# Kernel optimization log

Hardware: AMD Instinct MI355X
Metric: run time of the kernel (lower is better)

## Reference

```python
import jax, jax.numpy as jnp
import numpy as np

EPS = 1e-6
T, B, E, H, D, P = 1024, 4, 512, 8, 64, 64  # tgt_len, bsz, embed_dim, heads, head_dim, proj_dim


def setup_inputs() -> dict:
    key = jax.random.key(0)
    ks = jax.random.split(key, 8)
    wscale = (2.0 / (E + E)) ** 0.5  # xavier-ish, gain=init_scale**-0.5=1
    return {
        "x": jax.random.normal(ks[0], (T, B, E), jnp.float32),
        "random_matrices": jax.random.normal(ks[1], (H, P, D), jnp.float32),
        "Wq": jax.random.normal(ks[2], (E, E), jnp.float32) * wscale,
        "bq": jnp.zeros((E,), jnp.float32),
        "Wk": jax.random.normal(ks[3], (E, E), jnp.float32) * wscale,
        "bk": jnp.zeros((E,), jnp.float32),
        "Wv": jax.random.normal(ks[4], (E, E), jnp.float32) * wscale,
        "bv": jnp.zeros((E,), jnp.float32),
        "Wo": jax.random.normal(ks[5], (E, E), jnp.float32) * wscale,
        "bo": jnp.zeros((E,), jnp.float32),
    }


def _phi(x, rm, tau=1.0):
    # RFA trig random features: l2-normalize (scaled by 1/tau), project with
    # per-head random matrices, then [sin, cos] / sqrt(proj_dim).
    # x: [T,B,H,D], rm: [H,P,D] -> [T,B,H,2P]
    xn = x / (tau * jnp.maximum(jnp.linalg.norm(x, axis=-1, keepdims=True), EPS))
    proj = jnp.einsum('tbhd,hpd->tbhp', xn, rm)
    return jnp.concatenate([jnp.sin(proj), jnp.cos(proj)], axis=-1) * (P ** -0.5)


def reference(x, random_matrices, Wq, bq, Wk, bk, Wv, bv, Wo, bo):
    t, b, e = x.shape
    q = (x @ Wq.T + bq).reshape(t, b, H, D)
    k = (x @ Wk.T + bk).reshape(t, b, H, D)
    v = (x @ Wv.T + bv).reshape(t, b, H, D)

    pq = _phi(q, random_matrices)  # [T,B,H,2P]
    pk = _phi(k, random_matrices)  # [T,B,H,2P]

    K = 2 * P
    s0 = jnp.zeros((b, H, K, D), x.dtype)
    z0 = jnp.zeros((b, H, K), x.dtype)

    def step(carry, inp):
        s, z = carry
        pq_t, pk_t, v_t = inp  # [B,H,K], [B,H,K], [B,H,D]
        s = s + pk_t[..., :, None] * v_t[..., None, :]   # outer(phi_k, v)
        z = z + pk_t
        qs = jnp.einsum('bhk,bhkd->bhd', pq_t, s)
        qz = jnp.maximum(jnp.einsum('bhk,bhk->bh', pq_t, z), EPS)
        return (s, z), qs / qz[..., None]

    _, attn = jax.lax.scan(step, (s0, z0), (pq, pk, v))  # attn: [T,B,H,D]
    attn = attn.reshape(t, b, e)
    return attn @ Wo.T + bo
```

## Files before the change

kernel.cpp:

```cpp
#include <hip/hip_runtime.h>

#define T_ 1024
#define B_ 4
#define E_ 512
#define H_ 8
#define D_ 64
#define P_ 64
#define K2 128
#define N_ (T_*B_)
#define CHK 64
#define NC (T_/CHK)
#define BH (B_*H_)
#define EPSV 1e-6f

typedef unsigned int uint;
typedef unsigned short ushort;
typedef short short8 __attribute__((ext_vector_type(8)));
typedef float f32x4 __attribute__((ext_vector_type(4)));

__device__ __forceinline__ float b2f(ushort u){ return __uint_as_float(((uint)u) << 16); }
__device__ __forceinline__ ushort f2b(float f){
  uint x = __float_as_uint(f);
  return (ushort)((x + 0x7fffu + ((x >> 16) & 1u)) >> 16);
}
__device__ __forceinline__ float lo16(uint u){ return __uint_as_float(u << 16); }
__device__ __forceinline__ float hi16(uint u){ return __uint_as_float(u & 0xffff0000u); }
__device__ __forceinline__ void st(float* p, float v){ *p = v; }
__device__ __forceinline__ void st(ushort* p, float v){ *p = f2b(v); }

__device__ __forceinline__ void gl16(const ushort* g, ushort* lds) {
  __builtin_amdgcn_global_load_lds(
      (const __attribute__((address_space(1))) uint*)g,
      (__attribute__((address_space(3))) uint*)lds, 16, 0, 0);
}

__global__ __launch_bounds__(256) void cast_kernel(
    const float* __restrict__ x, const float* __restrict__ wq, const float* __restrict__ wk,
    const float* __restrict__ wv, const float* __restrict__ wo, const float* __restrict__ rm,
    ushort* __restrict__ xb, ushort* __restrict__ wqb, ushort* __restrict__ wkb,
    ushort* __restrict__ wvb, ushort* __restrict__ wob, ushort* __restrict__ rmb)
{
  const float* src; ushort* dst; int n4;
  switch (blockIdx.y) {
    case 0:  src = x;  dst = xb;  n4 = N_ * E_ / 4; break;
    case 1:  src = wq; dst = wqb; n4 = E_ * E_ / 4; break;
    case 2:  src = wk; dst = wkb; n4 = E_ * E_ / 4; break;
    case 3:  src = wv; dst = wvb; n4 = E_ * E_ / 4; break;
    case 4:  src = wo; dst = wob; n4 = E_ * E_ / 4; break;
    default: src = rm; dst = rmb; n4 = H_ * P_ * D_ / 4; break;
  }
  const int stride = gridDim.x * 256;
  for (int i = blockIdx.x * 256 + threadIdx.x; i < n4; i += stride) {
    const float4 v = *(const float4*)(src + (size_t)i * 4);
    ushort4 o; o.x = f2b(v.x); o.y = f2b(v.y); o.z = f2b(v.z); o.w = f2b(v.w);
    *(ushort4*)(dst + (size_t)i * 4) = o;
  }
}

template<typename OutT>
__device__ __forceinline__ void gemm_tile(
    const ushort* __restrict__ A, const ushort* __restrict__ W,
    const float* __restrict__ bias, OutT* __restrict__ out,
    const int row0, const int col0)
{
  __shared__ ushort sA[128 * 32];
  __shared__ ushort sB[64 * 32];
  const int tid = threadIdx.x, w = tid >> 6, lane = tid & 63;
  const int lrow = lane >> 2, lk8 = (lane & 3) * 8;
  const ushort* gA = A + (size_t)(row0 + w * 16 + lrow) * E_ + lk8;
  const ushort* gB = W + (size_t)(col0 + w * 16 + lrow) * E_ + lk8;
  ushort* lA = sA + w * 512;
  ushort* lB = sB + w * 512;
  const int r = lane & 15, kg = lane >> 4, kq = kg * 8;
  f32x4 acc[4][4] = {};
  for (int k0 = 0; k0 < E_; k0 += 32) {
    gl16(gA + k0,             lA);
    gl16(gA + k0 + 32 * E_,   lA + 1024);
    gl16(gA + k0 + 64 * E_,   lA + 2048);
    gl16(gA + k0 + 96 * E_,   lA + 3072);
    gl16(gB + k0,             lB);
    gl16(gB + k0 + 32 * E_,   lB + 1024);
    __syncthreads();
    short8 af[4], bf[4];
    #pragma unroll
    for (int m = 0; m < 4; ++m) af[m] = *(const short8*)(sA + (w * 64 + m * 16 + r) * 32 + kq);
    #pragma unroll
    for (int n = 0; n < 4; ++n) bf[n] = *(const short8*)(sB + (n * 16 + r) * 32 + kq);
    #pragma unroll
    for (int m = 0; m < 4; ++m)
      #pragma unroll
      for (int n = 0; n < 4; ++n)
        acc[m][n] = __builtin_amdgcn_mfma_f32_16x16x32_bf16(af[m], bf[n], acc[m][n], 0, 0, 0);
    __syncthreads();
  }
  float bs[4];
  #pragma unroll
  for (int n = 0; n < 4; ++n) bs[n] = bias[col0 + n * 16 + r];
  #pragma unroll
  for (int m = 0; m < 4; ++m) {
    #pragma unroll
    for (int j = 0; j < 4; ++j) {
      const int row_g = row0 + w * 64 + m * 16 + kg * 4 + j;
      #pragma unroll
      for (int n = 0; n < 4; ++n)
        st(out + (size_t)row_g * E_ + col0 + n * 16 + r, acc[m][n][j] + bs[n]);
    }
  }
}

__global__ __launch_bounds__(128) void gemm_qkv_kernel(
    const ushort* __restrict__ A,
    const ushort* __restrict__ wq, const ushort* __restrict__ wk, const ushort* __restrict__ wv,
    const float* __restrict__ bq, const float* __restrict__ bk, const float* __restrict__ bv,
    ushort* __restrict__ qb, ushort* __restrict__ kb, ushort* __restrict__ vb)
{
  const ushort* W; const float* bias; ushort* dst;
  if (blockIdx.z == 0)      { W = wq; bias = bq; dst = qb; }
  else if (blockIdx.z == 1) { W = wk; bias = bk; dst = kb; }
  else                      { W = wv; bias = bv; dst = vb; }
  gemm_tile<ushort>(A, W, bias, dst, blockIdx.x * 128, blockIdx.y * 64);
}

__global__ __launch_bounds__(128) void gemm_out_kernel(
    const ushort* __restrict__ A, const ushort* __restrict__ W,
    const float* __restrict__ bias, float* __restrict__ out)
{
  gemm_tile<float>(A, W, bias, out, blockIdx.x * 128, blockIdx.y * 64);
}

__global__ __launch_bounds__(256) void phi_kernel(
    const ushort* __restrict__ qb, const ushort* __restrict__ kb,
    const ushort* __restrict__ rmb, ushort* __restrict__ pq, ushort* __restrict__ pk)
{
  __shared__ ushort xq[64][72];
  __shared__ ushort rms[64][72];
  __shared__ float inv_s[64];
  const int tid = threadIdx.x;
  const int h = blockIdx.y;
  const ushort* src = blockIdx.z ? kb : qb;
  ushort* dst = blockIdx.z ? pk : pq;
  const int n0 = blockIdx.x * 64;
  const int row = tid >> 2, seg = (tid & 3) * 16;
  {
    const ushort* gq = src + (size_t)(n0 + row) * E_ + h * D_ + seg;
    const ushort* gr = rmb + ((size_t)h * P_ + row) * D_ + seg;
    const uint4 q0 = *(const uint4*)(gq);
    const uint4 q1 = *(const uint4*)(gq + 8);
    *(uint4*)(&xq[row][seg])      = q0;
    *(uint4*)(&xq[row][seg + 8])  = q1;
    *(uint4*)(&rms[row][seg])     = *(const uint4*)(gr);
    *(uint4*)(&rms[row][seg + 8]) = *(const uint4*)(gr + 8);
    float s2 = 0.f;
    const uint* qw = (const uint*)&q0;
    #pragma unroll
    for (int i = 0; i < 4; ++i) { const float a = lo16(qw[i]), b = hi16(qw[i]); s2 += a*a + b*b; }
    const uint* qw1 = (const uint*)&q1;
    #pragma unroll
    for (int i = 0; i < 4; ++i) { const float a = lo16(qw1[i]), b = hi16(qw1[i]); s2 += a*a + b*b; }
    s2 += __shfl_xor(s2, 1, 64);
    s2 += __shfl_xor(s2, 2, 64);
    if ((tid & 3) == 0) inv_s[row] = 1.0f / fmaxf(sqrtf(s2), EPSV);
  }
  __syncthreads();
  const int w = tid >> 6, lane = tid & 63;
  const int r = lane & 15, kg = lane >> 4;
  const int m0 = w * 16;
  f32x4 acc[4] = {};
  #pragma unroll
  for (int k0 = 0; k0 < D_; k0 += 32) {
    const short8 a = *(const short8*)(&xq[m0 + r][k0 + kg * 8]);
    #pragma unroll
    for (int nt = 0; nt < 4; ++nt) {
      const short8 bfr = *(const short8*)(&rms[nt * 16 + r][k0 + kg * 8]);
      acc[nt] = __builtin_amdgcn_mfma_f32_16x16x32_bf16(a, bfr, acc[nt], 0, 0, 0);
    }
  }
  #pragma unroll
  for (int j = 0; j < 4; ++j) {
    const int rr = m0 + kg * 4 + j;
    const float inv = inv_s[rr];
    const size_t base = ((size_t)(n0 + rr) * H_ + h) * K2;
    #pragma unroll
    for (int nt = 0; nt < 4; ++nt) {
      const int p = nt * 16 + r;
      const float proj = acc[nt][j] * inv;
      dst[base + p]      = f2b(__sinf(proj) * 0.125f);
      dst[base + 64 + p] = f2b(__cosf(proj) * 0.125f);
    }
  }
}

__global__ __launch_bounds__(256) void chunk_sum_kernel(
    const ushort* __restrict__ pk, const ushort* __restrict__ v,
    float* __restrict__ cS, float* __restrict__ cz)
{
  const int c = blockIdx.x, bh = blockIdx.y, b = bh >> 3, h = bh & 7;
  __shared__ ushort pkT[K2][88];
  __shared__ ushort vT[D_][88];
  const int tid = threadIdx.x;
  for (int i = tid; i < CHK * 16; i += 256) {
    const int tt = i >> 4, k8 = (i & 15) * 8;
    const int n = (c * CHK + tt) * B_ + b;
    const ushort4 u0 = *(const ushort4*)(pk + ((size_t)n * H_ + h) * K2 + k8);
    const ushort4 u1 = *(const ushort4*)(pk + ((size_t)n * H_ + h) * K2 + k8 + 4);
    pkT[k8+0][tt] = u0.x; pkT[k8+1][tt] = u0.y; pkT[k8+2][tt] = u0.z; pkT[k8+3][tt] = u0.w;
    pkT[k8+4][tt] = u1.x; pkT[k8+5][tt] = u1.y; pkT[k8+6][tt] = u1.z; pkT[k8+7][tt] = u1.w;
  }
  for (int i = tid; i < CHK * 16; i += 256) {
    const int tt = i >> 4, d4 = (i & 15) * 4;
    const int n = (c * CHK + tt) * B_ + b;
    const ushort4 u = *(const ushort4*)(v + (size_t)n * E_ + h * D_ + d4);
    vT[d4+0][tt] = u.x; vT[d4+1][tt] = u.y; vT[d4+2][tt] = u.z; vT[d4+3][tt] = u.w;
  }
  __syncthreads();
  const int w = tid >> 6, lane = tid & 63;
  const int r = lane & 15, kb = lane >> 4;
  const int m0 = w * 32;
  f32x4 acc[2][4] = {};
  #pragma unroll
  for (int k0 = 0; k0 < CHK; k0 += 32) {
    const short8 a0 = *(const short8*)(&pkT[m0 + r][k0 + kb * 8]);
    const short8 a1 = *(const short8*)(&pkT[m0 + 16 + r][k0 + kb * 8]);
    #pragma unroll
    for (int nt = 0; nt < 4; ++nt) {
      const short8 bv = *(const short8*)(&vT[nt * 16 + r][k0 + kb * 8]);
      acc[0][nt] = __builtin_amdgcn_mfma_f32_16x16x32_bf16(a0, bv, acc[0][nt], 0, 0, 0);
      acc[1][nt] = __builtin_amdgcn_mfma_f32_16x16x32_bf16(a1, bv, acc[1][nt], 0, 0, 0);
    }
  }
  float* So = cS + (size_t)(c * BH + bh) * (K2 * D_);
  #pragma unroll
  for (int mt = 0; mt < 2; ++mt)
    #pragma unroll
    for (int nt = 0; nt < 4; ++nt)
      #pragma unroll
      for (int j = 0; j < 4; ++j)
        So[(m0 + mt * 16 + kb * 4 + j) * D_ + nt * 16 + r] = acc[mt][nt][j];
  if (tid < K2) {
    float zacc = 0.f;
    #pragma unroll
    for (int i2 = 0; i2 < CHK / 2; ++i2) {
      const uint u = *(const uint*)(&pkT[tid][i2 * 2]);
      zacc += lo16(u) + hi16(u);
    }
    cz[(size_t)(c * BH + bh) * K2 + tid] = zacc;
  }
}

__global__ __launch_bounds__(256) void prefix_kernel(
    float* __restrict__ cS, float* __restrict__ cz)
{
  const int gid = blockIdx.x * 256 + threadIdx.x;
  const int bh = gid >> 13, rem = gid & 8191;
  float run = 0.f;
  #pragma unroll
  for (int c = 0; c < NC; ++c) {
    float* p = cS + (((size_t)(c * BH + bh)) << 13) + rem;
    const float t = *p; *p = run; run += t;
  }
  if (gid < BH * K2) {
    const int zbh = gid >> 7, k2 = gid & 127;
    float rz = 0.f;
    #pragma unroll
    for (int c = 0; c < NC; ++c) {
      float* pz = cz + (size_t)(c * BH + zbh) * K2 + k2;
      const float t = *pz; *pz = rz; rz += t;
    }
  }
}

__global__ __launch_bounds__(256) void chunk_out_kernel(
    const ushort* __restrict__ pq, const ushort* __restrict__ pkg,
    const ushort* __restrict__ v, const float* __restrict__ Sp,
    const float* __restrict__ zp, ushort* __restrict__ attn)
{
  const int c = blockIdx.x, bh = blockIdx.y, b = bh >> 3, h = bh & 7;
  __shared__ ushort pq_s[CHK][136];
  __shared__ ushort pk_s[CHK][136];
  __shared__ ushort SpT_s[D_][136];
  __shared__ ushort vT_s[D_][88];
  __shared__ ushort Am_s[CHK][88];
  __shared__ float zps[K2];
  __shared__ float dens_s[CHK];
  __shared__ float inv_s[CHK];
  const int tid = threadIdx.x;
  for (int i = tid; i < CHK * 16; i += 256) {
    const int tt = i >> 4, k8 = (i & 15) * 8;
    const int n = (c * CHK + tt) * B_ + b;
    const size_t off = ((size_t)n * H_ + h) * K2 + k8;
    *(uint4*)(&pq_s[tt][k8]) = *(const uint4*)(pq + off);
    *(uint4*)(&pk_s[tt][k8]) = *(const uint4*)(pkg + off);
  }
  for (int i = tid; i < CHK * 16; i += 256) {
    const int tt = i >> 4, d4 = (i & 15) * 4;
    const int n = (c * CHK + tt) * B_ + b;
    const ushort4 u = *(const ushort4*)(v + (size_t)n * E_ + h * D_ + d4);
    vT_s[d4+0][tt] = u.x; vT_s[d4+1][tt] = u.y; vT_s[d4+2][tt] = u.z; vT_s[d4+3][tt] = u.w;
  }
  const float* Spb = Sp + (size_t)(c * BH + bh) * (K2 * D_);
  for (int i = tid; i < K2 * 16; i += 256) {
    const int k2 = i >> 4, d4 = (i & 15) * 4;
    const float4 s = *(const float4*)(Spb + k2 * D_ + d4);
    SpT_s[d4+0][k2] = f2b(s.x); SpT_s[d4+1][k2] = f2b(s.y);
    SpT_s[d4+2][k2] = f2b(s.z); SpT_s[d4+3][k2] = f2b(s.w);
  }
  if (tid < K2) zps[tid] = zp[(size_t)(c * BH + bh) * K2 + tid];
  __syncthreads();

  const int w = tid >> 6, lane = tid & 63;
  const int r = lane & 15, kb = lane >> 4;
  const int m0 = w * 16;
  f32x4 accA[4] = {};
  #pragma unroll
  for (int k0 = 0; k0 < K2; k0 += 32) {
    const short8 aq = *(const short8*)(&pq_s[m0 + r][k0 + kb * 8]);
    #pragma unroll
    for (int nt = 0; nt < 4; ++nt) {
      const short8 bk = *(const short8*)(&pk_s[nt * 16 + r][k0 + kb * 8]);
      accA[nt] = __builtin_amdgcn_mfma_f32_16x16x32_bf16(aq, bk, accA[nt], 0, 0, 0);
    }
  }
  float rs[4] = {0.f, 0.f, 0.f, 0.f};
  #pragma unroll
  for (int nt = 0; nt < 4; ++nt) {
    #pragma unroll
    for (int j = 0; j < 4; ++j) {
      const int row = kb * 4 + j, col = nt * 16 + r;
      float a = accA[nt][j];
      a = (col <= m0 + row) ? a : 0.f;
      rs[j] += a;
      Am_s[m0 + row][col] = f2b(a);
    }
  }
  #pragma unroll
  for (int off = 1; off < 16; off <<= 1) {
    rs[0] += __shfl_xor(rs[0], off, 64);
    rs[1] += __shfl_xor(rs[1], off, 64);
    rs[2] += __shfl_xor(rs[2], off, 64);
    rs[3] += __shfl_xor(rs[3], off, 64);
  }
  if (r == 0) {
    #pragma unroll
    for (int j = 0; j < 4; ++j) dens_s[m0 + kb * 4 + j] = rs[j];
  }
  f32x4 accO[4] = {};
  #pragma unroll
  for (int k0 = 0; k0 < CHK; k0 += 32) {
    const short8 aa = *(const short8*)(&Am_s[m0 + r][k0 + kb * 8]);
    #pragma unroll
    for (int nt = 0; nt < 4; ++nt) {
      const short8 bv = *(const short8*)(&vT_s[nt * 16 + r][k0 + kb * 8]);
      accO[nt] = __builtin_amdgcn_mfma_f32_16x16x32_bf16(aa, bv, accO[nt], 0, 0, 0);
    }
  }
  #pragma unroll
  for (int k0 = 0; k0 < K2; k0 += 32) {
    const short8 aq = *(const short8*)(&pq_s[m0 + r][k0 + kb * 8]);
    #pragma unroll
    for (int nt = 0; nt < 4; ++nt) {
      const short8 bs = *(const short8*)(&SpT_s[nt * 16 + r][k0 + kb * 8]);
      accO[nt] = __builtin_amdgcn_mfma_f32_16x16x32_bf16(aq, bs, accO[nt], 0, 0, 0);
    }
  }
  {
    const int t_loc = m0 + (lane >> 2), seg = lane & 3;
    float qz = 0.f;
    #pragma unroll
    for (int ii = 0; ii < 16; ++ii) {
      const uint u = *(const uint*)(&pq_s[t_loc][seg * 32 + ii * 2]);
      qz += lo16(u) * zps[seg * 32 + ii * 2] + hi16(u) * zps[seg * 32 + ii * 2 + 1];
    }
    qz += __shfl_xor(qz, 1, 64);
    qz += __shfl_xor(qz, 2, 64);
    if (seg == 0) inv_s[t_loc] = 1.0f / fmaxf(dens_s[t_loc] + qz, EPSV);
  }
  #pragma unroll
  for (int j = 0; j < 4; ++j) {
    const int row = m0 + kb * 4 + j;
    const float inv = inv_s[row];
    const int n = (c * CHK + row) * B_ + b;
    ushort* op = attn + (size_t)n * E_ + h * D_;
    #pragma unroll
    for (int nt = 0; nt < 4; ++nt) op[nt * 16 + r] = f2b(accO[nt][j] * inv);
  }
}

extern "C" void kernel_launch(void* const* d_in, const int* in_sizes, int n_in,
                              void* d_out, int out_size, void* d_ws, size_t ws_size,
                              hipStream_t stream) {
  const float* x  = (const float*)d_in[0];
  const float* rm = (const float*)d_in[1];
  const float* Wq = (const float*)d_in[2];
  const float* bq = (const float*)d_in[3];
  const float* Wk = (const float*)d_in[4];
  const float* bk = (const float*)d_in[5];
  const float* Wv = (const float*)d_in[6];
  const float* bv = (const float*)d_in[7];
  const float* Wo = (const float*)d_in[8];
  const float* bo = (const float*)d_in[9];
  float* out = (float*)d_out;

  ushort* xb  = (ushort*)d_ws;
  ushort* wqb = xb + (size_t)N_ * E_;
  ushort* wkb = wqb + (size_t)E_ * E_;
  ushort* wvb = wkb + (size_t)E_ * E_;
  ushort* wob = wvb + (size_t)E_ * E_;
  ushort* rmb = wob + (size_t)E_ * E_;
  ushort* qb  = rmb + (size_t)H_ * P_ * D_;
  ushort* kb  = qb + (size_t)N_ * E_;
  ushort* vb  = kb + (size_t)N_ * E_;
  ushort* pqb = vb + (size_t)N_ * E_;
  ushort* pkb = pqb + (size_t)N_ * H_ * K2;
  ushort* attnb = pkb + (size_t)N_ * H_ * K2;
  float* cS = (float*)(attnb + (size_t)N_ * E_);
  float* cz = cS + (size_t)NC * BH * K2 * D_;

  cast_kernel<<<dim3(512, 6), dim3(256), 0, stream>>>(
      x, Wq, Wk, Wv, Wo, rm, xb, wqb, wkb, wvb, wob, rmb);
  gemm_qkv_kernel<<<dim3(N_ / 128, E_ / 64, 3), dim3(128), 0, stream>>>(
      xb, wqb, wkb, wvb, bq, bk, bv, qb, kb, vb);
  phi_kernel<<<dim3(N_ / 64, H_, 2), dim3(256), 0, stream>>>(qb, kb, rmb, pqb, pkb);
  chunk_sum_kernel<<<dim3(NC, BH), dim3(256), 0, stream>>>(pkb, vb, cS, cz);
  prefix_kernel<<<dim3(1024), dim3(256), 0, stream>>>(cS, cz);
  chunk_out_kernel<<<dim3(NC, BH), dim3(256), 0, stream>>>(pqb, pkb, vb, cS, cz, attnb);
  gemm_out_kernel<<<dim3(N_ / 128, E_ / 64), dim3(128), 0, stream>>>(attnb, wob, bo, out);
}
```

Before: 68.29 us.

## Fuse chunk-sum, prefix and chunk-output into one sequential per-head scan kernel

```diff
diff --git a/kernel.cpp b/kernel.cpp
--- a/kernel.cpp
+++ b/kernel.cpp
@@ -190,198 +190,152 @@
   }
 }
 
-__global__ __launch_bounds__(256) void chunk_sum_kernel(
-    const ushort* __restrict__ pk, const ushort* __restrict__ v,
-    float* __restrict__ cS, float* __restrict__ cz)
-{
-  const int c = blockIdx.x, bh = blockIdx.y, b = bh >> 3, h = bh & 7;
-  __shared__ ushort pkT[K2][88];
-  __shared__ ushort vT[D_][88];
-  const int tid = threadIdx.x;
-  for (int i = tid; i < CHK * 16; i += 256) {
-    const int tt = i >> 4, k8 = (i & 15) * 8;
-    const int n = (c * CHK + tt) * B_ + b;
-    const ushort4 u0 = *(const ushort4*)(pk + ((size_t)n * H_ + h) * K2 + k8);
-    const ushort4 u1 = *(const ushort4*)(pk + ((size_t)n * H_ + h) * K2 + k8 + 4);
-    pkT[k8+0][tt] = u0.x; pkT[k8+1][tt] = u0.y; pkT[k8+2][tt] = u0.z; pkT[k8+3][tt] = u0.w;
-    pkT[k8+4][tt] = u1.x; pkT[k8+5][tt] = u1.y; pkT[k8+6][tt] = u1.z; pkT[k8+7][tt] = u1.w;
-  }
-  for (int i = tid; i < CHK * 16; i += 256) {
-    const int tt = i >> 4, d4 = (i & 15) * 4;
-    const int n = (c * CHK + tt) * B_ + b;
-    const ushort4 u = *(const ushort4*)(v + (size_t)n * E_ + h * D_ + d4);
-    vT[d4+0][tt] = u.x; vT[d4+1][tt] = u.y; vT[d4+2][tt] = u.z; vT[d4+3][tt] = u.w;
-  }
-  __syncthreads();
-  const int w = tid >> 6, lane = tid & 63;
-  const int r = lane & 15, kb = lane >> 4;
-  const int m0 = w * 32;
-  f32x4 acc[2][4] = {};
-  #pragma unroll
-  for (int k0 = 0; k0 < CHK; k0 += 32) {
-    const short8 a0 = *(const short8*)(&pkT[m0 + r][k0 + kb * 8]);
-    const short8 a1 = *(const short8*)(&pkT[m0 + 16 + r][k0 + kb * 8]);
-    #pragma unroll
-    for (int nt = 0; nt < 4; ++nt) {
-      const short8 bv = *(const short8*)(&vT[nt * 16 + r][k0 + kb * 8]);
-      acc[0][nt] = __builtin_amdgcn_mfma_f32_16x16x32_bf16(a0, bv, acc[0][nt], 0, 0, 0);
-      acc[1][nt] = __builtin_amdgcn_mfma_f32_16x16x32_bf16(a1, bv, acc[1][nt], 0, 0, 0);
-    }
-  }
-  float* So = cS + (size_t)(c * BH + bh) * (K2 * D_);
-  #pragma unroll
-  for (int mt = 0; mt < 2; ++mt)
-    #pragma unroll
-    for (int nt = 0; nt < 4; ++nt)
-      #pragma unroll
-      for (int j = 0; j < 4; ++j)
-        So[(m0 + mt * 16 + kb * 4 + j) * D_ + nt * 16 + r] = acc[mt][nt][j];
-  if (tid < K2) {
-    float zacc = 0.f;
-    #pragma unroll
-    for (int i2 = 0; i2 < CHK / 2; ++i2) {
-      const uint u = *(const uint*)(&pkT[tid][i2 * 2]);
-      zacc += lo16(u) + hi16(u);
-    }
-    cz[(size_t)(c * BH + bh) * K2 + tid] = zacc;
-  }
-}
-
-__global__ __launch_bounds__(256) void prefix_kernel(
-    float* __restrict__ cS, float* __restrict__ cz)
-{
-  const int gid = blockIdx.x * 256 + threadIdx.x;
-  const int bh = gid >> 13, rem = gid & 8191;
-  float run = 0.f;
-  #pragma unroll
-  for (int c = 0; c < NC; ++c) {
-    float* p = cS + (((size_t)(c * BH + bh)) << 13) + rem;
-    const float t = *p; *p = run; run += t;
-  }
-  if (gid < BH * K2) {
-    const int zbh = gid >> 7, k2 = gid & 127;
-    float rz = 0.f;
-    #pragma unroll
-    for (int c = 0; c < NC; ++c) {
-      float* pz = cz + (size_t)(c * BH + zbh) * K2 + k2;
-      const float t = *pz; *pz = rz; rz += t;
-    }
-  }
-}
-
-__global__ __launch_bounds__(256) void chunk_out_kernel(
+__global__ __launch_bounds__(256) void scan_kernel(
     const ushort* __restrict__ pq, const ushort* __restrict__ pkg,
-    const ushort* __restrict__ v, const float* __restrict__ Sp,
-    const float* __restrict__ zp, ushort* __restrict__ attn)
-{
-  const int c = blockIdx.x, bh = blockIdx.y, b = bh >> 3, h = bh & 7;
+    const ushort* __restrict__ v, ushort* __restrict__ attn)
+{
+  const int bh = blockIdx.x, dh = blockIdx.y;
+  const int b = bh >> 3, h = bh & 7;
   __shared__ ushort pq_s[CHK][136];
   __shared__ ushort pk_s[CHK][136];
-  __shared__ ushort SpT_s[D_][136];
-  __shared__ ushort vT_s[D_][88];
+  __shared__ ushort pkT[K2][88];
+  __shared__ ushort vT[32][88];
+  __shared__ ushort SpT[32][136];
   __shared__ ushort Am_s[CHK][88];
-  __shared__ float zps[K2];
+  __shared__ float zrun[K2];
   __shared__ float dens_s[CHK];
   __shared__ float inv_s[CHK];
   const int tid = threadIdx.x;
-  for (int i = tid; i < CHK * 16; i += 256) {
-    const int tt = i >> 4, k8 = (i & 15) * 8;
-    const int n = (c * CHK + tt) * B_ + b;
-    const size_t off = ((size_t)n * H_ + h) * K2 + k8;
-    *(uint4*)(&pq_s[tt][k8]) = *(const uint4*)(pq + off);
-    *(uint4*)(&pk_s[tt][k8]) = *(const uint4*)(pkg + off);
-  }
-  for (int i = tid; i < CHK * 16; i += 256) {
-    const int tt = i >> 4, d4 = (i & 15) * 4;
-    const int n = (c * CHK + tt) * B_ + b;
-    const ushort4 u = *(const ushort4*)(v + (size_t)n * E_ + h * D_ + d4);
-    vT_s[d4+0][tt] = u.x; vT_s[d4+1][tt] = u.y; vT_s[d4+2][tt] = u.z; vT_s[d4+3][tt] = u.w;
-  }
-  const float* Spb = Sp + (size_t)(c * BH + bh) * (K2 * D_);
-  for (int i = tid; i < K2 * 16; i += 256) {
-    const int k2 = i >> 4, d4 = (i & 15) * 4;
-    const float4 s = *(const float4*)(Spb + k2 * D_ + d4);
-    SpT_s[d4+0][k2] = f2b(s.x); SpT_s[d4+1][k2] = f2b(s.y);
-    SpT_s[d4+2][k2] = f2b(s.z); SpT_s[d4+3][k2] = f2b(s.w);
-  }
-  if (tid < K2) zps[tid] = zp[(size_t)(c * BH + bh) * K2 + tid];
-  __syncthreads();
-
   const int w = tid >> 6, lane = tid & 63;
   const int r = lane & 15, kb = lane >> 4;
   const int m0 = w * 16;
-  f32x4 accA[4] = {};
-  #pragma unroll
-  for (int k0 = 0; k0 < K2; k0 += 32) {
-    const short8 aq = *(const short8*)(&pq_s[m0 + r][k0 + kb * 8]);
+  for (int i = tid; i < 32 * 136; i += 256) ((ushort*)SpT)[i] = 0;
+  if (tid < K2) zrun[tid] = 0.f;
+  f32x4 Sfrag[2][2] = {};
+
+  for (int c = 0; c < NC; ++c) {
+    __syncthreads();
+    for (int i = tid; i < CHK * 16; i += 256) {
+      const int tt = i >> 4, k8 = (i & 15) * 8;
+      const int n = (c * CHK + tt) * B_ + b;
+      const size_t off = ((size_t)n * H_ + h) * K2 + k8;
+      *(uint4*)(&pq_s[tt][k8]) = *(const uint4*)(pq + off);
+      const uint4 uk = *(const uint4*)(pkg + off);
+      *(uint4*)(&pk_s[tt][k8]) = uk;
+      const ushort* us = (const ushort*)&uk;
+      #pragma unroll
+      for (int e = 0; e < 8; ++e) pkT[k8 + e][tt] = us[e];
+    }
+    for (int i = tid; i < CHK * 4; i += 256) {
+      const int tt = i >> 2, d8 = (i & 3) * 8;
+      const int n = (c * CHK + tt) * B_ + b;
+      const uint4 u = *(const uint4*)(v + (size_t)n * E_ + h * D_ + dh * 32 + d8);
+      const ushort* us = (const ushort*)&u;
+      #pragma unroll
+      for (int e = 0; e < 8; ++e) vT[d8 + e][tt] = us[e];
+    }
+    __syncthreads();
+    f32x4 accA[4] = {};
+    #pragma unroll
+    for (int k0 = 0; k0 < K2; k0 += 32) {
+      const short8 aq = *(const short8*)(&pq_s[m0 + r][k0 + kb * 8]);
+      #pragma unroll
+      for (int nt = 0; nt < 4; ++nt) {
+        const short8 bk = *(const short8*)(&pk_s[nt * 16 + r][k0 + kb * 8]);
+        accA[nt] = __builtin_amdgcn_mfma_f32_16x16x32_bf16(aq, bk, accA[nt], 0, 0, 0);
+      }
+    }
+    float rs[4] = {0.f, 0.f, 0.f, 0.f};
     #pragma unroll
     for (int nt = 0; nt < 4; ++nt) {
-      const short8 bk = *(const short8*)(&pk_s[nt * 16 + r][k0 + kb * 8]);
-      accA[nt] = __builtin_amdgcn_mfma_f32_16x16x32_bf16(aq, bk, accA[nt], 0, 0, 0);
-    }
-  }
-  float rs[4] = {0.f, 0.f, 0.f, 0.f};
-  #pragma unroll
-  for (int nt = 0; nt < 4; ++nt) {
+      #pragma unroll
+      for (int j = 0; j < 4; ++j) {
+        const int row = kb * 4 + j, col = nt * 16 + r;
+        float a = accA[nt][j];
+        a = (col <= m0 + row) ? a : 0.f;
+        rs[j] += a;
+        Am_s[m0 + row][col] = f2b(a);
+      }
+    }
+    #pragma unroll
+    for (int off = 1; off < 16; off <<= 1) {
+      rs[0] += __shfl_xor(rs[0], off, 64);
+      rs[1] += __shfl_xor(rs[1], off, 64);
+      rs[2] += __shfl_xor(rs[2], off, 64);
+      rs[3] += __shfl_xor(rs[3], off, 64);
+    }
+    if (r == 0) {
+      #pragma unroll
+      for (int j = 0; j < 4; ++j) dens_s[m0 + kb * 4 + j] = rs[j];
+    }
+    f32x4 accO[2] = {};
+    #pragma unroll
+    for (int k0 = 0; k0 < CHK; k0 += 32) {
+      const short8 aa = *(const short8*)(&Am_s[m0 + r][k0 + kb * 8]);
+      #pragma unroll
+      for (int nt = 0; nt < 2; ++nt) {
+        const short8 bv = *(const short8*)(&vT[nt * 16 + r][k0 + kb * 8]);
+        accO[nt] = __builtin_amdgcn_mfma_f32_16x16x32_bf16(aa, bv, accO[nt], 0, 0, 0);
+      }
+    }
+    #pragma unroll
+    for (int k0 = 0; k0 < K2; k0 += 32) {
+      const short8 aq = *(const short8*)(&pq_s[m0 + r][k0 + kb * 8]);
+      #pragma unroll
+      for (int nt = 0; nt < 2; ++nt) {
+        const short8 bs = *(const short8*)(&SpT[nt * 16 + r][k0 + kb * 8]);
+        accO[nt] = __builtin_amdgcn_mfma_f32_16x16x32_bf16(aq, bs, accO[nt], 0, 0, 0);
+      }
+    }
+    {
+      const int t_loc = m0 + (lane >> 2), seg = lane & 3;
+      float qz = 0.f;
+      #pragma unroll
+      for (int ii = 0; ii < 16; ++ii) {
+        const uint u = *(const uint*)(&pq_s[t_loc][seg * 32 + ii * 2]);
+        qz += lo16(u) * zrun[seg * 32 + ii * 2] + hi16(u) * zrun[seg * 32 + ii * 2 + 1];
+      }
+      qz += __shfl_xor(qz, 1, 64);
+      qz += __shfl_xor(qz, 2, 64);
+      if (seg == 0) inv_s[t_loc] = 1.0f / fmaxf(dens_s[t_loc] + qz, EPSV);
+    }
     #pragma unroll
     for (int j = 0; j < 4; ++j) {
-      const int row = kb * 4 + j, col = nt * 16 + r;
-      float a = accA[nt][j];
-      a = (col <= m0 + row) ? a : 0.f;
-      rs[j] += a;
-      Am_s[m0 + row][col] = f2b(a);
-    }
-  }
-  #pragma unroll
-  for (int off = 1; off < 16; off <<= 1) {
-    rs[0] += __shfl_xor(rs[0], off, 64);
-    rs[1] += __shfl_xor(rs[1], off, 64);
-    rs[2] += __shfl_xor(rs[2], off, 64);
-    rs[3] += __shfl_xor(rs[3], off, 64);
-  }
-  if (r == 0) {
-    #pragma unroll
-    for (int j = 0; j < 4; ++j) dens_s[m0 + kb * 4 + j] = rs[j];
-  }
-  f32x4 accO[4] = {};
-  #pragma unroll
-  for (int k0 = 0; k0 < CHK; k0 += 32) {
-    const short8 aa = *(const short8*)(&Am_s[m0 + r][k0 + kb * 8]);
-    #pragma unroll
-    for (int nt = 0; nt < 4; ++nt) {
-      const short8 bv = *(const short8*)(&vT_s[nt * 16 + r][k0 + kb * 8]);
-      accO[nt] = __builtin_amdgcn_mfma_f32_16x16x32_bf16(aa, bv, accO[nt], 0, 0, 0);
-    }
-  }
-  #pragma unroll
-  for (int k0 = 0; k0 < K2; k0 += 32) {
-    const short8 aq = *(const short8*)(&pq_s[m0 + r][k0 + kb * 8]);
-    #pragma unroll
-    for (int nt = 0; nt < 4; ++nt) {
-      const short8 bs = *(const short8*)(&SpT_s[nt * 16 + r][k0 + kb * 8]);
-      accO[nt] = __builtin_amdgcn_mfma_f32_16x16x32_bf16(aq, bs, accO[nt], 0, 0, 0);
-    }
-  }
-  {
-    const int t_loc = m0 + (lane >> 2), seg = lane & 3;
-    float qz = 0.f;
-    #pragma unroll
-    for (int ii = 0; ii < 16; ++ii) {
-      const uint u = *(const uint*)(&pq_s[t_loc][seg * 32 + ii * 2]);
-      qz += lo16(u) * zps[seg * 32 + ii * 2] + hi16(u) * zps[seg * 32 + ii * 2 + 1];
-    }
-    qz += __shfl_xor(qz, 1, 64);
-    qz += __shfl_xor(qz, 2, 64);
-    if (seg == 0) inv_s[t_loc] = 1.0f / fmaxf(dens_s[t_loc] + qz, EPSV);
-  }
-  #pragma unroll
-  for (int j = 0; j < 4; ++j) {
-    const int row = m0 + kb * 4 + j;
-    const float inv = inv_s[row];
-    const int n = (c * CHK + row) * B_ + b;
-    ushort* op = attn + (size_t)n * E_ + h * D_;
-    #pragma unroll
-    for (int nt = 0; nt < 4; ++nt) op[nt * 16 + r] = f2b(accO[nt][j] * inv);
+      const int row = m0 + kb * 4 + j;
+      const float inv = inv_s[row];
+      const int n = (c * CHK + row) * B_ + b;
+      ushort* op = attn + (size_t)n * E_ + h * D_ + dh * 32;
+      #pragma unroll
+      for (int nt = 0; nt < 2; ++nt) op[nt * 16 + r] = f2b(accO[nt][j] * inv);
+    }
+    __syncthreads();
+    #pragma unroll
+    for (int k0 = 0; k0 < CHK; k0 += 32) {
+      const short8 a0 = *(const short8*)(&pkT[w * 32 + r][k0 + kb * 8]);
+      const short8 a1 = *(const short8*)(&pkT[w * 32 + 16 + r][k0 + kb * 8]);
+      #pragma unroll
+      for (int nt = 0; nt < 2; ++nt) {
+        const short8 bv = *(const short8*)(&vT[nt * 16 + r][k0 + kb * 8]);
+        Sfrag[0][nt] = __builtin_amdgcn_mfma_f32_16x16x32_bf16(a0, bv, Sfrag[0][nt], 0, 0, 0);
+        Sfrag[1][nt] = __builtin_amdgcn_mfma_f32_16x16x32_bf16(a1, bv, Sfrag[1][nt], 0, 0, 0);
+      }
+    }
+    #pragma unroll
+    for (int m = 0; m < 2; ++m)
+      #pragma unroll
+      for (int nt = 0; nt < 2; ++nt)
+        #pragma unroll
+        for (int j = 0; j < 4; ++j)
+          SpT[nt * 16 + r][w * 32 + m * 16 + kb * 4 + j] = f2b(Sfrag[m][nt][j]);
+    if (tid < K2) {
+      float z = 0.f;
+      #pragma unroll
+      for (int i2 = 0; i2 < CHK / 2; ++i2) {
+        const uint u = *(const uint*)(&pkT[tid][i2 * 2]);
+        z += lo16(u) + hi16(u);
+      }
+      zrun[tid] += z;
+    }
   }
 }
 
@@ -412,16 +366,12 @@
   ushort* pqb = vb + (size_t)N_ * E_;
   ushort* pkb = pqb + (size_t)N_ * H_ * K2;
   ushort* attnb = pkb + (size_t)N_ * H_ * K2;
-  float* cS = (float*)(attnb + (size_t)N_ * E_);
-  float* cz = cS + (size_t)NC * BH * K2 * D_;
 
   cast_kernel<<<dim3(512, 6), dim3(256), 0, stream>>>(
       x, Wq, Wk, Wv, Wo, rm, xb, wqb, wkb, wvb, wob, rmb);
   gemm_qkv_kernel<<<dim3(N_ / 128, E_ / 64, 3), dim3(128), 0, stream>>>(
       xb, wqb, wkb, wvb, bq, bk, bv, qb, kb, vb);
   phi_kernel<<<dim3(N_ / 64, H_, 2), dim3(256), 0, stream>>>(qb, kb, rmb, pqb, pkb);
-  chunk_sum_kernel<<<dim3(NC, BH), dim3(256), 0, stream>>>(pkb, vb, cS, cz);
-  prefix_kernel<<<dim3(1024), dim3(256), 0, stream>>>(cS, cz);
-  chunk_out_kernel<<<dim3(NC, BH), dim3(256), 0, stream>>>(pqb, pkb, vb, cS, cz, attnb);
+  scan_kernel<<<dim3(BH, 2), dim3(256), 0, stream>>>(pqb, pkb, vb, attnb);
   gemm_out_kernel<<<dim3(N_ / 128, E_ / 64), dim3(128), 0, stream>>>(attnb, wob, bo, out);
 }
```

New measurement: 119.4 us. +74.8%, slower.
